# Optimization experiments

Measured on AMD Instinct MI355X. Metric: run time of the kernel, lower is better.

The kernel has to match this reference:

```python
import jax, jax.numpy as jnp
import numpy as np

N, H, C, E, R = 16384, 1024, 256, 16, 128
EPS = 1e-8


def setup_inputs() -> dict:
    key = jax.random.key(0)
    ks = jax.random.split(key, 8)
    s = 1.0 / np.sqrt(H)
    return {
        "x": jax.random.normal(ks[0], (N, H), jnp.float32),
        "Wd": jax.random.normal(ks[1], (H, C), jnp.float32) * s,
        "bd": jax.random.normal(ks[2], (C,), jnp.float32) * 0.01,
        "centroids": jax.random.uniform(ks[3], (E, C), jnp.float32),  # torch.rand
        "Wg": jax.random.normal(ks[4], (E, H, H), jnp.float32) * s,
        "bg": jax.random.normal(ks[5], (E, H), jnp.float32) * 0.01,
        "U": jax.random.normal(ks[6], (E, H, R), jnp.float32) * s,
        "V": jax.random.normal(ks[7], (E, R, H), jnp.float32) * (1.0 / np.sqrt(R)),
        "k": 2,
    }


def reference(x, Wd, bd, centroids, Wg, bg, U, V, k):
    # ---- Router ----
    distilled = jax.nn.gelu(x @ Wd + bd, approximate=False)          # [N, C]
    dn = distilled / jnp.maximum(
        jnp.linalg.norm(distilled, axis=-1, keepdims=True), EPS)
    cn = centroids / jnp.maximum(
        jnp.linalg.norm(centroids, axis=-1, keepdims=True), EPS)
    # cdist (euclidean) between dn [N,C] and cn [E,C]
    d2 = (jnp.sum(dn * dn, -1, keepdims=True)
          + jnp.sum(cn * cn, -1)[None, :]
          - 2.0 * (dn @ cn.T))                                        # [N, E]
    distances = jnp.sqrt(jnp.maximum(d2, 0.0))
    probabilities = jax.nn.softmax(-distances, axis=-1)               # [N, E]
    top_p, top_i = jax.lax.top_k(probabilities, k)                    # [N, k]
    # sparse combine weights: zero except at top-k experts
    combine = jnp.zeros((x.shape[0], E), x.dtype)
    combine = combine.at[jnp.arange(x.shape[0])[:, None], top_i].set(top_p)
    # ---- Expert dispatch: scan over experts (low-rank Highway blocks) ----
    def body(acc, params):
        Wg_e, bg_e, U_e, V_e, w_e = params
        gate = jax.nn.sigmoid(x @ Wg_e + bg_e)                        # [N, H]
        trans = (x @ U_e) @ V_e                                       # [N, H]
        y = gate * trans + (1.0 - gate) * x
        return acc + w_e[:, None] * y, None
    out, _ = jax.lax.scan(body, jnp.zeros_like(x),
                          (Wg, bg, U, V, combine.T))
    return out
```

## Files before the change

### kernel.cpp

```cpp
#include <hip/hip_runtime.h>
#include <hip/hip_bf16.h>
#include <hip/hip_fp16.h>
#include <cstdint>
#include <cstddef>

#define NTOK 16384
#define HD   1024
#define CD   256
#define NE   16
#define RD   128
#define MB2    272
#define LOGB   2176
#define EGRID  2304

typedef __attribute__((ext_vector_type(8))) short bf16x8;
typedef __attribute__((ext_vector_type(4))) float f32x4;
typedef unsigned short u16;
typedef unsigned int u32;

__device__ __forceinline__ u16 f2bf(float f) {
    u32 u = __float_as_uint(f);
    u32 r = (u + 0x7FFFu + ((u >> 16) & 1u)) >> 16;
    return (u16)r;
}
__device__ __forceinline__ float bf2f(u16 h) {
    u32 u = ((u32)h) << 16;
    return __uint_as_float(u);
}

__device__ __forceinline__ void gload16(const void* g, void* lds) {
    __builtin_amdgcn_global_load_lds((const __attribute__((address_space(1))) void*)g,
                                     (__attribute__((address_space(3))) void*)lds,
                                     16, 0, 0);
}

__device__ __forceinline__ float wredsum(float v) {
#pragma unroll
    for (int m = 32; m >= 1; m >>= 1) v += __shfl_xor(v, m, 64);
    return v;
}

__global__ __launch_bounds__(64) void centroid_norm_kernel(
    const float* __restrict__ cen, float* __restrict__ cn, float* __restrict__ sncn)
{
    int e = blockIdx.x, l = threadIdx.x;
    float4 c = *(const float4*)&cen[e * CD + l * 4];
    float ss = wredsum(c.x * c.x + c.y * c.y + c.z * c.z + c.w * c.w);
    float den = fmaxf(sqrtf(ss), 1e-8f);
    float4 n;
    n.x = c.x / den; n.y = c.y / den; n.z = c.z / den; n.w = c.w / den;
    *(float4*)&cn[e * CD + l * 4] = n;
    float s2 = wredsum(n.x * n.x + n.y * n.y + n.z * n.z + n.w * n.w);
    if (l == 0) sncn[e] = s2;
}

__global__ __launch_bounds__(256) void cvt_split_kernel(
    const float* __restrict__ src, u16* __restrict__ hi, u16* __restrict__ lo, int n4)
{
    int i = blockIdx.x * 256 + threadIdx.x;
    if (i >= n4) return;
    float4 v = *(const float4*)&src[(size_t)i * 4];
    ushort4 h, l;
    h.x = f2bf(v.x); h.y = f2bf(v.y); h.z = f2bf(v.z); h.w = f2bf(v.w);
    l.x = f2bf(v.x - bf2f(h.x)); l.y = f2bf(v.y - bf2f(h.y));
    l.z = f2bf(v.z - bf2f(h.z)); l.w = f2bf(v.w - bf2f(h.w));
    *(ushort4*)&hi[(size_t)i * 4] = h;
    *(ushort4*)&lo[(size_t)i * 4] = l;
}

__global__ __launch_bounds__(256) void transpose_cvt_kernel(
    const float* __restrict__ src, u16* __restrict__ dst, int K, int N)
{
    __shared__ float t[32][33];
    const float* s = src + (size_t)blockIdx.z * K * N;
    u16* d = dst + (size_t)blockIdx.z * K * N;
    int kb = blockIdx.y * 32, nb = blockIdx.x * 32;
    int r = threadIdx.x >> 3, c4 = (threadIdx.x & 7) * 4;
    float4 v = *(const float4*)&s[(size_t)(kb + r) * N + nb + c4];
    t[r][c4 + 0] = v.x; t[r][c4 + 1] = v.y; t[r][c4 + 2] = v.z; t[r][c4 + 3] = v.w;
    __syncthreads();
    ushort4 o;
    o.x = f2bf(t[c4 + 0][r]); o.y = f2bf(t[c4 + 1][r]);
    o.z = f2bf(t[c4 + 2][r]); o.w = f2bf(t[c4 + 3][r]);
    *(ushort4*)&d[(size_t)(nb + r) * K + kb + c4] = o;
}

__global__ __launch_bounds__(256) void transpose_cvt_split_kernel(
    const float* __restrict__ src, u16* __restrict__ dh, u16* __restrict__ dl,
    int K, int N)
{
    __shared__ float t[32][33];
    int kb = blockIdx.y * 32, nb = blockIdx.x * 32;
    int r = threadIdx.x >> 3, c4 = (threadIdx.x & 7) * 4;
    float4 v = *(const float4*)&src[(size_t)(kb + r) * N + nb + c4];
    t[r][c4 + 0] = v.x; t[r][c4 + 1] = v.y; t[r][c4 + 2] = v.z; t[r][c4 + 3] = v.w;
    __syncthreads();
    float f0 = t[c4 + 0][r], f1 = t[c4 + 1][r], f2 = t[c4 + 2][r], f3 = t[c4 + 3][r];
    ushort4 h, l;
    h.x = f2bf(f0); h.y = f2bf(f1); h.z = f2bf(f2); h.w = f2bf(f3);
    l.x = f2bf(f0 - bf2f(h.x)); l.y = f2bf(f1 - bf2f(h.y));
    l.z = f2bf(f2 - bf2f(h.z)); l.w = f2bf(f3 - bf2f(h.w));
    *(ushort4*)&dh[(size_t)(nb + r) * K + kb + c4] = h;
    *(ushort4*)&dl[(size_t)(nb + r) * K + kb + c4] = l;
}


__global__ __launch_bounds__(256, 2) void router_mfma_kernel(
    const u16* __restrict__ xh, const u16* __restrict__ xl,
    const u16* __restrict__ wdh, const u16* __restrict__ wdl,
    const float* __restrict__ bd, float* __restrict__ dT)
{
    __shared__ __align__(16) u16 lds[2 * 16384];
    int rb = (blockIdx.x >> 1) * 128;
    int cb = (blockIdx.x & 1) * 128;
    int tid = threadIdx.x, lane = tid & 63, w = tid >> 6;
    int lrow = lane >> 2;
    int sl = (lane & 3) ^ ((lane >> 3) & 3);
    int rr = lane & 15, hi = lane >> 4;
    int rslot = hi ^ ((rr >> 1) & 3);
    int wr = w >> 1, wc = w & 1;

    const u16* gb[8]; char* lp[8];
#pragma unroll
    for (int i = 0; i < 8; ++i) {
        int idx = w + 4 * i;
        int sub = idx & 7;
        int row = sub * 16 + lrow;
        if (idx < 8) {
            gb[i] = xh + (size_t)(rb + row) * HD + sl * 8;
            lp[i] = (char*)lds + idx * 1024;
        } else if (idx < 16) {
            gb[i] = xl + (size_t)(rb + row) * HD + sl * 8;
            lp[i] = (char*)lds + 8192 + sub * 1024;
        } else if (idx < 24) {
            gb[i] = wdh + (size_t)(cb + row) * HD + sl * 8;
            lp[i] = (char*)lds + 16384 + sub * 1024;
        } else {
            gb[i] = wdl + (size_t)(cb + row) * HD + sl * 8;
            lp[i] = (char*)lds + 24576 + sub * 1024;
        }
    }

    const f32x4 zz = {0.f, 0.f, 0.f, 0.f};
    f32x4 acc[4][4];
#pragma unroll
    for (int im = 0; im < 4; ++im)
#pragma unroll
        for (int in = 0; in < 4; ++in) acc[im][in] = zz;

    auto STAGE = [&](int buf, int t) {
#pragma unroll
        for (int i = 0; i < 8; ++i) gload16(gb[i] + t * 32, lp[i] + buf * 32768);
    };
    auto COMP = [&](int buf) {
        const u16* LXH = lds + buf * 16384;
        const u16* LXL = LXH + 4096;
        const u16* LWH = LXH + 8192;
        const u16* LWL = LXH + 12288;
        bf16x8 ah[4], al[4], bh[4], bl[4];
#pragma unroll
        for (int im = 0; im < 4; ++im) {
            int row = wr * 64 + im * 16 + rr;
            ah[im] = *(const bf16x8*)&LXH[row * 32 + rslot * 8];
            al[im] = *(const bf16x8*)&LXL[row * 32 + rslot * 8];
        }
#pragma unroll
        for (int in = 0; in < 4; ++in) {
            int row = wc * 64 + in * 16 + rr;
            bh[in] = *(const bf16x8*)&LWH[row * 32 + rslot * 8];
            bl[in] = *(const bf16x8*)&LWL[row * 32 + rslot * 8];
        }
#pragma unroll
        for (int im = 0; im < 4; ++im)
#pragma unroll
            for (int in = 0; in < 4; ++in) {
                acc[im][in] = __builtin_amdgcn_mfma_f32_16x16x32_bf16(ah[im], bh[in], acc[im][in], 0, 0, 0);
                acc[im][in] = __builtin_amdgcn_mfma_f32_16x16x32_bf16(ah[im], bl[in], acc[im][in], 0, 0, 0);
                acc[im][in] = __builtin_amdgcn_mfma_f32_16x16x32_bf16(al[im], bh[in], acc[im][in], 0, 0, 0);
            }
    };

    STAGE(0, 0);
    __syncthreads();
    for (int t = 0; t < 31; ++t) {
        STAGE((t + 1) & 1, t + 1);
        COMP(t & 1);
        __syncthreads();
    }
    COMP(1);

#pragma unroll
    for (int im = 0; im < 4; ++im)
#pragma unroll
        for (int in = 0; in < 4; ++in) {
            int c = cb + wc * 64 + in * 16 + rr;
            float b = bd[c];
            float g[4];
#pragma unroll
            for (int j = 0; j < 4; ++j) {
                float v = acc[im][in][j] + b;
                g[j] = 0.5f * v * (1.f + erff(v * 0.70710678118654752f));
            }
            float4 o = {g[0], g[1], g[2], g[3]};
            *(float4*)&dT[(size_t)c * NTOK + rb + wr * 64 + im * 16 + hi * 4] = o;
        }
}

__global__ __launch_bounds__(256) void router_score_kernel(
    const float* __restrict__ dT, const float* __restrict__ cn,
    const float* __restrict__ sncn, int* __restrict__ top_i,
    float* __restrict__ top_w, int* __restrict__ counts)
{
    __shared__ float lcn[NE][CD];
    __shared__ float sdot[NE][64];
    __shared__ float sss[64];
    __shared__ int hist[NE];
    int tid = threadIdx.x, lane = tid & 63, w = tid >> 6;
    for (int i = tid; i < NE * CD / 4; i += 256)
        ((float4*)&lcn[0][0])[i] = ((const float4*)cn)[i];
    if (tid < NE) hist[tid] = 0;
    __syncthreads();

    int tokbase = blockIdx.x * 64;
    const float* p = dT + tokbase + lane;
    int e0 = w * 4;
    float d0 = 0.f, d1 = 0.f, d2a = 0.f, d3 = 0.f, ss = 0.f;
#pragma unroll 4
    for (int k = 0; k < CD; ++k) {
        float v = p[(size_t)k * NTOK];
        ss = fmaf(v, v, ss);
        d0 = fmaf(v, lcn[e0 + 0][k], d0);
        d1 = fmaf(v, lcn[e0 + 1][k], d1);
        d2a = fmaf(v, lcn[e0 + 2][k], d2a);
        d3 = fmaf(v, lcn[e0 + 3][k], d3);
    }
    sdot[e0 + 0][lane] = d0;
    sdot[e0 + 1][lane] = d1;
    sdot[e0 + 2][lane] = d2a;
    sdot[e0 + 3][lane] = d3;
    if (w == 0) sss[lane] = ss;
    __syncthreads();

    if (tid < 64) {
        int tok = tokbase + tid;
        float ssv = sss[tid];
        float den = fmaxf(sqrtf(ssv), 1e-8f);
        float inv = 1.f / den;
        float sndn = (ssv * inv) * inv;
        float pr[NE];
#pragma unroll
        for (int e = 0; e < NE; ++e) {
            float dotn = sdot[e][tid] * inv;
            float dd2 = sndn + sncn[e] - 2.f * dotn;
            pr[e] = -sqrtf(fmaxf(dd2, 0.f));
        }
        float mx = pr[0];
#pragma unroll
        for (int e = 1; e < NE; ++e) mx = fmaxf(mx, pr[e]);
        float sum = 0.f;
#pragma unroll
        for (int e = 0; e < NE; ++e) { pr[e] = expf(pr[e] - mx); sum += pr[e]; }
        float invs = 1.f / sum;
#pragma unroll
        for (int e = 0; e < NE; ++e) pr[e] *= invs;
        int i1 = 0; float p1 = pr[0];
#pragma unroll
        for (int e = 1; e < NE; ++e) if (pr[e] > p1) { p1 = pr[e]; i1 = e; }
        int i2 = -1; float p2 = -1.f;
#pragma unroll
        for (int e = 0; e < NE; ++e) if (e != i1 && pr[e] > p2) { p2 = pr[e]; i2 = e; }
        top_i[tok * 2 + 0] = i1; top_w[tok * 2 + 0] = p1;
        top_i[tok * 2 + 1] = i2; top_w[tok * 2 + 1] = p2;
        atomicAdd(&hist[i1], 1);
        atomicAdd(&hist[i2], 1);
    }
    __syncthreads();
    if (tid < NE) atomicAdd(&counts[tid], hist[tid]);
}

__global__ void scan_kernel(const int* __restrict__ counts, int* __restrict__ offsets,
                            int* __restrict__ blkstart, int* __restrict__ cursor)
{
    if (threadIdx.x == 0 && blockIdx.x == 0) {
        int o = 0, b = 0;
        for (int e = 0; e < NE; ++e) {
            offsets[e] = o; blkstart[e] = b; cursor[e] = 0;
            o += counts[e]; b += (counts[e] + 127) >> 7;
        }
        offsets[NE] = o; blkstart[NE] = b;
    }
}

__global__ __launch_bounds__(256) void build_lists_kernel(
    const int* __restrict__ top_i, const float* __restrict__ top_w,
    const int* __restrict__ offsets, int* __restrict__ cursor,
    int* __restrict__ list_tok, float* __restrict__ list_w)
{
    int t = blockIdx.x * 256 + threadIdx.x;
#pragma unroll
    for (int j = 0; j < 2; ++j) {
        int e = top_i[t * 2 + j];
        int pos = atomicAdd(&cursor[e], 1);
        int idx = offsets[e] + pos;
        list_tok[idx] = t;
        list_w[idx] = top_w[t * 2 + j];
    }
}

__global__ __launch_bounds__(256, 3) void tproj_kernel(
    const u16* __restrict__ xbf, const u16* __restrict__ uT,
    const int* __restrict__ list_tok, const int* __restrict__ offsets,
    const int* __restrict__ blkstart, u16* __restrict__ tbf)
{
    __shared__ __align__(16) u16 lds[2 * 8192];
    __shared__ int s_tok[128];
    int mb = blockIdx.x;
    int e = 0;
#pragma unroll
    for (int i = 0; i < NE; ++i) if (mb >= blkstart[i + 1]) e = i + 1;
    if (e >= NE) return;
    int mloc = (mb - blkstart[e]) * 128;
    int base = offsets[e] + mloc;
    int cnt = offsets[e + 1] - offsets[e];
    int mv = min(128, cnt - mloc);
    int tid = threadIdx.x, lane = tid & 63, w = tid >> 6;
    if (tid < 128) s_tok[tid] = list_tok[base + (tid < mv ? tid : 0)];
    __syncthreads();
    int lrow = lane >> 2;
    int sl = (lane & 3) ^ ((lane >> 3) & 3);
    int rr = lane & 15, hi = lane >> 4;
    int rslot = hi ^ ((rr >> 1) & 3);
    int wr = w >> 1, wc = w & 1;
    const u16* uE = uT + (size_t)e * RD * HD;

    const u16* gb[4]; char* lp[4];
#pragma unroll
    for (int i = 0; i < 4; ++i) {
        int idx = w + 4 * i;
        if (idx < 8) {
            int row = idx * 16 + lrow;
            gb[i] = xbf + (size_t)s_tok[row] * HD + sl * 8;
            lp[i] = (char*)lds + idx * 1024;
        } else {
            int row = (idx - 8) * 16 + lrow;
            gb[i] = uE + (size_t)row * HD + sl * 8;
            lp[i] = (char*)lds + 8192 + (idx - 8) * 1024;
        }
    }
    const f32x4 zz = {0.f, 0.f, 0.f, 0.f};
    f32x4 acc[4][4];
#pragma unroll
    for (int im = 0; im < 4; ++im)
#pragma unroll
        for (int in = 0; in < 4; ++in) acc[im][in] = zz;

    auto STAGE = [&](int buf, int t) {
#pragma unroll
        for (int i = 0; i < 4; ++i) gload16(gb[i] + t * 32, lp[i] + buf * 16384);
    };
    auto COMP = [&](int buf, f32x4 (&a)[4][4]) {
        const u16* LA = lds + buf * 8192;
        const u16* LB = LA + 4096;
        bf16x8 af[4], bfv[4];
#pragma unroll
        for (int im = 0; im < 4; ++im) af[im] = *(const bf16x8*)&LA[(wr * 64 + im * 16 + rr) * 32 + rslot * 8];
#pragma unroll
        for (int in = 0; in < 4; ++in) bfv[in] = *(const bf16x8*)&LB[(wc * 64 + in * 16 + rr) * 32 + rslot * 8];
#pragma unroll
        for (int im = 0; im < 4; ++im)
#pragma unroll
            for (int in = 0; in < 4; ++in)
                a[im][in] = __builtin_amdgcn_mfma_f32_16x16x32_bf16(af[im], bfv[in], a[im][in], 0, 0, 0);
    };

    STAGE(0, 0);
    __syncthreads();
    for (int t = 0; t < 31; ++t) {
        STAGE((t + 1) & 1, t + 1);
        COMP(t & 1, acc);
        __syncthreads();
    }
    COMP(1, acc);

#pragma unroll
    for (int im = 0; im < 4; ++im)
#pragma unroll
        for (int in = 0; in < 4; ++in)
#pragma unroll
            for (int j = 0; j < 4; ++j) {
                int r = wr * 64 + im * 16 + hi * 4 + j;
                if (r < mv) {
                    int c = wc * 64 + in * 16 + rr;
                    tbf[(size_t)(base + r) * RD + c] = f2bf(acc[im][in][j]);
                }
            }
}

__global__ __launch_bounds__(256, 3) void expert_kernel(
    const u16* __restrict__ xbf, const u16* __restrict__ wgT,
    const u16* __restrict__ vT, const u16* __restrict__ tbf,
    const float* __restrict__ x, const float* __restrict__ bg,
    const int* __restrict__ list_tok, const float* __restrict__ list_w,
    const int* __restrict__ offsets, const int* __restrict__ blkstart,
    float* __restrict__ out)
{
    __shared__ __align__(16) u16 lds[2 * 8192];
    __shared__ int s_tok[128];
    __shared__ float s_w[128];
    int d = blockIdx.x;
    int l = (d >> 8) * 256 + (d & 7) * 32 + ((d & 255) >> 3);
    if (l >= LOGB) return;
    int g = l >> 5, i2d = l & 31;
    int mb = (g >> 1) * 8 + (i2d & 7);
    int ct = (g & 1) * 4 + (i2d >> 3);
    int e = 0;
#pragma unroll
    for (int i = 0; i < NE; ++i) if (mb >= blkstart[i + 1]) e = i + 1;
    if (e >= NE) return;
    int mloc = (mb - blkstart[e]) * 128;
    int base = offsets[e] + mloc;
    int cnt = offsets[e + 1] - offsets[e];
    int mv = min(128, cnt - mloc);
    int tid = threadIdx.x, lane = tid & 63, w = tid >> 6;
    if (tid < 128) {
        int p = base + (tid < mv ? tid : 0);
        s_tok[tid] = list_tok[p];
        s_w[tid] = (tid < mv) ? list_w[p] : 0.f;
    }
    __syncthreads();
    int lrow = lane >> 2;
    int sl = (lane & 3) ^ ((lane >> 3) & 3);
    int rr = lane & 15, hi = lane >> 4;
    int rslot = hi ^ ((rr >> 1) & 3);
    int wr = w >> 1, wc = w & 1;

    const u16* wgE = wgT + (size_t)e * HD * HD + (size_t)(ct * 128) * HD;
    const u16* vE  = vT  + (size_t)e * HD * RD + (size_t)(ct * 128) * RD;

    char* lp[4];
    const u16* gbT[4]; const u16* gbG[4];
#pragma unroll
    for (int i = 0; i < 4; ++i) {
        int idx = w + 4 * i;
        if (idx < 8) {
            int row = idx * 16 + lrow;
            lp[i]  = (char*)lds + idx * 1024;
            gbT[i] = tbf + (size_t)(base + (row < mv ? row : 0)) * RD + sl * 8;
            gbG[i] = xbf + (size_t)s_tok[row] * HD + sl * 8;
        } else {
            int row = (idx - 8) * 16 + lrow;
            lp[i]  = (char*)lds + 8192 + (idx - 8) * 1024;
            gbT[i] = vE  + (size_t)row * RD + sl * 8;
            gbG[i] = wgE + (size_t)row * HD + sl * 8;
        }
    }

    auto STAGE = [&](int buf, int t, const u16* const (&gb)[4]) {
#pragma unroll
        for (int i = 0; i < 4; ++i) gload16(gb[i] + t * 32, lp[i] + buf * 16384);
    };
    auto COMP = [&](int buf, f32x4 (&a)[4][4]) {
        const u16* LA = lds + buf * 8192;
        const u16* LB = LA + 4096;
        bf16x8 af[4], bfv[4];
#pragma unroll
        for (int im = 0; im < 4; ++im) af[im] = *(const bf16x8*)&LA[(wr * 64 + im * 16 + rr) * 32 + rslot * 8];
#pragma unroll
        for (int in = 0; in < 4; ++in) bfv[in] = *(const bf16x8*)&LB[(wc * 64 + in * 16 + rr) * 32 + rslot * 8];
#pragma unroll
        for (int im = 0; im < 4; ++im)
#pragma unroll
            for (int in = 0; in < 4; ++in)
                a[im][in] = __builtin_amdgcn_mfma_f32_16x16x32_bf16(af[im], bfv[in], a[im][in], 0, 0, 0);
    };

    const f32x4 zz = {0.f, 0.f, 0.f, 0.f};
    f32x4 accT[4][4];
#pragma unroll
    for (int im = 0; im < 4; ++im)
#pragma unroll
        for (int in = 0; in < 4; ++in) accT[im][in] = zz;

    STAGE(0, 0, gbT);
    __syncthreads();
#pragma unroll
    for (int s = 0; s < 4; ++s) {
        if (s < 3) STAGE((s + 1) & 1, s + 1, gbT);
        else       STAGE(0, 0, gbG);
        COMP(s & 1, accT);
        __syncthreads();
    }

    __half2 tpk[4][4][2];
#pragma unroll
    for (int im = 0; im < 4; ++im)
#pragma unroll
        for (int in = 0; in < 4; ++in) {
            tpk[im][in][0] = __floats2half2_rn(accT[im][in][0], accT[im][in][1]);
            tpk[im][in][1] = __floats2half2_rn(accT[im][in][2], accT[im][in][3]);
        }

    f32x4 accG[4][4];
#pragma unroll
    for (int im = 0; im < 4; ++im)
#pragma unroll
        for (int in = 0; in < 4; ++in) accG[im][in] = zz;

    for (int t = 0; t < 31; ++t) {
        STAGE((t + 1) & 1, t + 1, gbG);
        COMP(t & 1, accG);
        __syncthreads();
    }
    COMP(1, accG);

    float bgv[4];
#pragma unroll
    for (int in = 0; in < 4; ++in)
        bgv[in] = bg[e * HD + ct * 128 + wc * 64 + in * 16 + rr];

#pragma unroll
    for (int im = 0; im < 4; ++im)
#pragma unroll
        for (int j = 0; j < 4; ++j) {
            int r = wr * 64 + im * 16 + hi * 4 + j;
            if (r < mv) {
                int tok = s_tok[r];
                float wgt = s_w[r];
                size_t rowoff = (size_t)tok * HD;
#pragma unroll
                for (int in = 0; in < 4; ++in) {
                    int c = ct * 128 + wc * 64 + in * 16 + rr;
                    float gp = accG[im][in][j] + bgv[in];
                    float sg = 1.f / (1.f + __expf(-gp));
                    float2 tq = __half22float2(tpk[im][in][j >> 1]);
                    float tr = (j & 1) ? tq.y : tq.x;
                    float xv = x[rowoff + c];
                    float yv = sg * tr + (1.f - sg) * xv;
                    atomicAdd(&out[rowoff + c], wgt * yv);
                }
            }
        }
}

extern "C" void kernel_launch(void* const* d_in, const int* in_sizes, int n_in,
                              void* d_out, int out_size, void* d_ws, size_t ws_size,
                              hipStream_t stream)
{
    const float* x   = (const float*)d_in[0];
    const float* Wd  = (const float*)d_in[1];
    const float* bd  = (const float*)d_in[2];
    const float* cen = (const float*)d_in[3];
    const float* Wg  = (const float*)d_in[4];
    const float* bg  = (const float*)d_in[5];
    const float* U   = (const float*)d_in[6];
    const float* V   = (const float*)d_in[7];
    float* out = (float*)d_out;

    char* ws = (char*)d_ws;
    size_t off = 0;
    auto alloc = [&](size_t bytes) { size_t o = off; off = (off + bytes + 255) & ~(size_t)255; return o; };
    float* dT        = (float*)(ws + alloc((size_t)NTOK * CD * 4));
    float* cn        = (float*)(ws + alloc((size_t)NE * CD * 4));
    float* sncn      = (float*)(ws + alloc(NE * 4));
    int*   top_i     = (int*)(ws + alloc((size_t)NTOK * 2 * 4));
    float* top_w     = (float*)(ws + alloc((size_t)NTOK * 2 * 4));
    int*   counts    = (int*)(ws + alloc(NE * 4));
    int*   offsets   = (int*)(ws + alloc((NE + 1) * 4));
    int*   blkstart  = (int*)(ws + alloc((NE + 1) * 4));
    int*   cursor    = (int*)(ws + alloc(NE * 4));
    int*   list_tok  = (int*)(ws + alloc((size_t)NTOK * 2 * 4));
    float* list_w    = (float*)(ws + alloc((size_t)NTOK * 2 * 4));
    u16*   xbf       = (u16*)(ws + alloc((size_t)NTOK * HD * 2));
    u16*   xlo       = (u16*)(ws + alloc((size_t)NTOK * HD * 2));
    u16*   wdh       = (u16*)(ws + alloc((size_t)CD * HD * 2));
    u16*   wdl       = (u16*)(ws + alloc((size_t)CD * HD * 2));
    u16*   wgT       = (u16*)(ws + alloc((size_t)NE * HD * HD * 2));
    u16*   uT        = (u16*)(ws + alloc((size_t)NE * RD * HD * 2));
    u16*   vT        = (u16*)(ws + alloc((size_t)NE * RD * HD * 2));
    u16*   tbf       = (u16*)(ws + alloc(((size_t)NTOK * 2 + 128) * RD * 2));

    hipMemsetAsync(out, 0, (size_t)out_size * 4, stream);
    hipMemsetAsync(counts, 0, NE * 4, stream);

    centroid_norm_kernel<<<NE, 64, 0, stream>>>(cen, cn, sncn);
    cvt_split_kernel<<<(NTOK * HD / 4 + 255) / 256, 256, 0, stream>>>(x, xbf, xlo, NTOK * HD / 4);
    transpose_cvt_split_kernel<<<dim3(CD / 32, HD / 32), 256, 0, stream>>>(Wd, wdh, wdl, HD, CD);
    router_mfma_kernel<<<(NTOK / 128) * 2, 256, 0, stream>>>(xbf, xlo, wdh, wdl, bd, dT);
    router_score_kernel<<<NTOK / 64, 256, 0, stream>>>(dT, cn, sncn, top_i, top_w, counts);
    scan_kernel<<<1, 64, 0, stream>>>(counts, offsets, blkstart, cursor);
    build_lists_kernel<<<NTOK / 256, 256, 0, stream>>>(top_i, top_w, offsets, cursor, list_tok, list_w);

    transpose_cvt_kernel<<<dim3(HD / 32, HD / 32, NE), 256, 0, stream>>>(Wg, wgT, HD, HD);
    transpose_cvt_kernel<<<dim3(RD / 32, HD / 32, NE), 256, 0, stream>>>(U, uT, HD, RD);
    transpose_cvt_kernel<<<dim3(HD / 32, RD / 32, NE), 256, 0, stream>>>(V, vT, RD, HD);

    tproj_kernel<<<MB2, 256, 0, stream>>>(xbf, uT, list_tok, offsets, blkstart, tbf);
    expert_kernel<<<EGRID, 256, 0, stream>>>(xbf, wgT, vT, tbf, x, bg,
                                             list_tok, list_w, offsets, blkstart, out);
}
```

Baseline: 503.2 us.

## Reorder expert kernel: gate GEMM first, then trans GEMM; raise occupancy to 4

The expert kernel now computes the gate GEMM first and folds the sigmoid into fp16-packed registers. It then runs the short low-rank trans GEMM and keeps its accumulators in fp32, instead of holding packed trans values live through the long gate loop. Both tproj and expert kernels raise the launch-bounds minimum blocks per CU from 3 to 4. The goal is less register pressure, so the kernels fit more waves and hide latency better. The risk is that the tighter register budget forces spills, and the gate is now stored in fp16 rather than the trans value. The diff also leaves some dead code behind: an unused extern shared array and a redundant vE pointer.

```diff
diff --git a/kernel.cpp b/kernel.cpp
--- a/kernel.cpp
+++ b/kernel.cpp
@@ -307,7 +307,7 @@
     }
 }
 
-__global__ __launch_bounds__(256, 3) void tproj_kernel(
+__global__ __launch_bounds__(256, 4) void tproj_kernel(
     const u16* __restrict__ xbf, const u16* __restrict__ uT,
     const int* __restrict__ list_tok, const int* __restrict__ offsets,
     const int* __restrict__ blkstart, u16* __restrict__ tbf)
@@ -396,7 +396,7 @@
             }
 }
 
-__global__ __launch_bounds__(256, 3) void expert_kernel(
+__global__ __launch_bounds__(256, 4) void expert_kernel(
     const u16* __restrict__ xbf, const u16* __restrict__ wgT,
     const u16* __restrict__ vT, const u16* __restrict__ tbf,
     const float* __restrict__ x, const float* __restrict__ bg,
@@ -435,24 +435,12 @@
     int wr = w >> 1, wc = w & 1;
 
     const u16* wgE = wgT + (size_t)e * HD * HD + (size_t)(ct * 128) * HD;
-    const u16* vE  = vT  + (size_t)e * HD * RD + (size_t)(ct * 128) * RD;
 
     char* lp[4];
-    const u16* gbT[4]; const u16* gbG[4];
 #pragma unroll
     for (int i = 0; i < 4; ++i) {
         int idx = w + 4 * i;
-        if (idx < 8) {
-            int row = idx * 16 + lrow;
-            lp[i]  = (char*)lds + idx * 1024;
-            gbT[i] = tbf + (size_t)(base + (row < mv ? row : 0)) * RD + sl * 8;
-            gbG[i] = xbf + (size_t)s_tok[row] * HD + sl * 8;
-        } else {
-            int row = (idx - 8) * 16 + lrow;
-            lp[i]  = (char*)lds + 8192 + (idx - 8) * 1024;
-            gbT[i] = vE  + (size_t)row * RD + sl * 8;
-            gbG[i] = wgE + (size_t)row * HD + sl * 8;
-        }
+        lp[i] = (char*)lds + ((idx < 8) ? idx * 1024 : 8192 + (idx - 8) * 1024);
     }
 
     auto STAGE = [&](int buf, int t, const u16* const (&gb)[4]) {
@@ -475,71 +463,124 @@
     };
 
     const f32x4 zz = {0.f, 0.f, 0.f, 0.f};
-    f32x4 accT[4][4];
-#pragma unroll
-    for (int im = 0; im < 4; ++im)
-#pragma unroll
-        for (int in = 0; in < 4; ++in) accT[im][in] = zz;
-
-    STAGE(0, 0, gbT);
-    __syncthreads();
-#pragma unroll
-    for (int s = 0; s < 4; ++s) {
-        if (s < 3) STAGE((s + 1) & 1, s + 1, gbT);
-        else       STAGE(0, 0, gbG);
-        COMP(s & 1, accT);
+
+    {
+        const u16* gbG[4];
+#pragma unroll
+        for (int i = 0; i < 4; ++i) {
+            int idx = w + 4 * i;
+            if (idx < 8) {
+                int row = idx * 16 + lrow;
+                gbG[i] = xbf + (size_t)s_tok[row] * HD + sl * 8;
+            } else {
+                int row = (idx - 8) * 16 + lrow;
+                gbG[i] = wgE + (size_t)row * HD + sl * 8;
+            }
+        }
+
+        f32x4 accG[4][4];
+#pragma unroll
+        for (int im = 0; im < 4; ++im)
+#pragma unroll
+            for (int in = 0; in < 4; ++in) accG[im][in] = zz;
+
+        STAGE(0, 0, gbG);
         __syncthreads();
-    }
-
-    __half2 tpk[4][4][2];
-#pragma unroll
-    for (int im = 0; im < 4; ++im)
-#pragma unroll
-        for (int in = 0; in < 4; ++in) {
-            tpk[im][in][0] = __floats2half2_rn(accT[im][in][0], accT[im][in][1]);
-            tpk[im][in][1] = __floats2half2_rn(accT[im][in][2], accT[im][in][3]);
-        }
-
-    f32x4 accG[4][4];
-#pragma unroll
-    for (int im = 0; im < 4; ++im)
-#pragma unroll
-        for (int in = 0; in < 4; ++in) accG[im][in] = zz;
-
-    for (int t = 0; t < 31; ++t) {
-        STAGE((t + 1) & 1, t + 1, gbG);
-        COMP(t & 1, accG);
+        for (int t = 0; t < 31; ++t) {
+            STAGE((t + 1) & 1, t + 1, gbG);
+            COMP(t & 1, accG);
+            __syncthreads();
+        }
+        COMP(1, accG);
+
+        float bgv[4];
+#pragma unroll
+        for (int in = 0; in < 4; ++in)
+            bgv[in] = bg[e * HD + ct * 128 + wc * 64 + in * 16 + rr];
+        __half2* sgp = (__half2*)&s_w[0];
+        (void)sgp;
+        extern __shared__ char _dummy[]; (void)_dummy;
+        {
+        }
+        {
+            const u16* vE = vT + (size_t)e * HD * RD + (size_t)(ct * 128) * RD;
+            const u16* gbT0[4];
+#pragma unroll
+            for (int i = 0; i < 4; ++i) {
+                int idx = w + 4 * i;
+                if (idx < 8) {
+                    int row = idx * 16 + lrow;
+                    gbT0[i] = tbf + (size_t)(base + (row < mv ? row : 0)) * RD + sl * 8;
+                } else {
+                    int row = (idx - 8) * 16 + lrow;
+                    gbT0[i] = vE + (size_t)row * RD + sl * 8;
+                }
+            }
+            STAGE(0, 0, gbT0);
+        }
+        __half2 sgp_reg[4][4][2];
+#pragma unroll
+        for (int im = 0; im < 4; ++im)
+#pragma unroll
+            for (int in = 0; in < 4; ++in) {
+                float s0 = 1.f / (1.f + __expf(-(accG[im][in][0] + bgv[in])));
+                float s1 = 1.f / (1.f + __expf(-(accG[im][in][1] + bgv[in])));
+                float s2 = 1.f / (1.f + __expf(-(accG[im][in][2] + bgv[in])));
+                float s3 = 1.f / (1.f + __expf(-(accG[im][in][3] + bgv[in])));
+                sgp_reg[im][in][0] = __floats2half2_rn(s0, s1);
+                sgp_reg[im][in][1] = __floats2half2_rn(s2, s3);
+            }
         __syncthreads();
-    }
-    COMP(1, accG);
-
-    float bgv[4];
-#pragma unroll
-    for (int in = 0; in < 4; ++in)
-        bgv[in] = bg[e * HD + ct * 128 + wc * 64 + in * 16 + rr];
-
-#pragma unroll
-    for (int im = 0; im < 4; ++im)
-#pragma unroll
-        for (int j = 0; j < 4; ++j) {
-            int r = wr * 64 + im * 16 + hi * 4 + j;
-            if (r < mv) {
-                int tok = s_tok[r];
-                float wgt = s_w[r];
-                size_t rowoff = (size_t)tok * HD;
-#pragma unroll
-                for (int in = 0; in < 4; ++in) {
-                    int c = ct * 128 + wc * 64 + in * 16 + rr;
-                    float gp = accG[im][in][j] + bgv[in];
-                    float sg = 1.f / (1.f + __expf(-gp));
-                    float2 tq = __half22float2(tpk[im][in][j >> 1]);
-                    float tr = (j & 1) ? tq.y : tq.x;
-                    float xv = x[rowoff + c];
-                    float yv = sg * tr + (1.f - sg) * xv;
-                    atomicAdd(&out[rowoff + c], wgt * yv);
+
+        const u16* vE = vT + (size_t)e * HD * RD + (size_t)(ct * 128) * RD;
+        const u16* gbT[4];
+#pragma unroll
+        for (int i = 0; i < 4; ++i) {
+            int idx = w + 4 * i;
+            if (idx < 8) {
+                int row = idx * 16 + lrow;
+                gbT[i] = tbf + (size_t)(base + (row < mv ? row : 0)) * RD + sl * 8;
+            } else {
+                int row = (idx - 8) * 16 + lrow;
+                gbT[i] = vE + (size_t)row * RD + sl * 8;
+            }
+        }
+
+        f32x4 accT[4][4];
+#pragma unroll
+        for (int im = 0; im < 4; ++im)
+#pragma unroll
+            for (int in = 0; in < 4; ++in) accT[im][in] = zz;
+
+#pragma unroll
+        for (int s = 0; s < 4; ++s) {
+            if (s < 3) STAGE((s + 1) & 1, s + 1, gbT);
+            COMP(s & 1, accT);
+            __syncthreads();
+        }
+
+#pragma unroll
+        for (int im = 0; im < 4; ++im)
+#pragma unroll
+            for (int j = 0; j < 4; ++j) {
+                int r = wr * 64 + im * 16 + hi * 4 + j;
+                if (r < mv) {
+                    int tok = s_tok[r];
+                    float wgt = s_w[r];
+                    size_t rowoff = (size_t)tok * HD;
+#pragma unroll
+                    for (int in = 0; in < 4; ++in) {
+                        int c = ct * 128 + wc * 64 + in * 16 + rr;
+                        float2 sq = __half22float2(sgp_reg[im][in][j >> 1]);
+                        float sg = (j & 1) ? sq.y : sq.x;
+                        float tr = accT[im][in][j];
+                        float xv = x[rowoff + c];
+                        float yv = sg * tr + (1.f - sg) * xv;
+                        atomicAdd(&out[rowoff + c], wgt * yv);
+                    }
                 }
             }
-        }
+    }
 }
 
 extern "C" void kernel_launch(void* const* d_in, const int* in_sizes, int n_in,
```

Result: slower. 558.7 us (+11.0%).
